# Kernel tuning notes

Hardware: AMD Instinct MI355X
Metric: run time of the kernel (lower is better)

Reference implementation:

```python
import jax, jax.numpy as jnp
import numpy as np

B, C, N, QK, VC, S = 64, 64, 256, 8, 32, 16
EPS = 1e-5
SCALE = float(np.sqrt(QK))  # qk_channel ** 0.5


def _bn(x, p):
    # eval-mode BatchNorm1d over [B, C, N]; p = [gamma, beta, mean, var]
    g, b, m, v = p
    return (x - m[None, :, None]) * (g * jax.lax.rsqrt(v + EPS))[None, :, None] + b[None, :, None]


def _conv1x1(w, x, b=None):
    y = jnp.einsum('oc,bcn->bon', w, x)
    return y if b is None else y + b[None, :, None]


def setup_inputs() -> dict:
    key = jax.random.key(0)
    ks = jax.random.split(key, 16)

    def w(k, o, i):
        return jax.random.normal(k, (o, i), jnp.float32) * (1.0 / np.sqrt(i))

    def bn_p(k, c):
        k1, k2, k3, k4 = jax.random.split(k, 4)
        return jnp.stack([
            jax.random.uniform(k1, (c,), jnp.float32) + 0.5,   # gamma
            jax.random.normal(k2, (c,), jnp.float32) * 0.1,    # beta
            jax.random.normal(k3, (c,), jnp.float32) * 0.1,    # running mean
            jax.random.uniform(k4, (c,), jnp.float32) + 0.5,   # running var (>0)
        ])

    x = jax.random.normal(ks[0], (B, C, N), jnp.float32)
    stroke_idx = jax.random.randint(ks[1], (B, N), 0, S, jnp.int32)
    stroke_idx = stroke_idx.at[:, -1].set(S - 1)  # guarantee max == S-1

    ga_q_w = w(ks[2], QK, C)
    sa_q_w = w(ks[3], QK, C)
    inp = {
        'x': x,
        'stroke_idx': stroke_idx,
        'n_strokes': S,
        'ga_q_w': ga_q_w,
        'ga_k_w': ga_q_w.copy(),  # k initialized as clone of q in source
        'ga_v_w': w(ks[4], VC, C),
        'ga_v_b': jax.random.normal(ks[5], (VC,), jnp.float32) * 0.01,
        'ga_bn_p': bn_p(ks[6], VC),
        'ga_lb_w': w(ks[7], VC, C),
        'ga_lb_bn_p': bn_p(ks[8], VC),
        'sa_q_w': sa_q_w,
        'sa_k_w': sa_q_w.copy(),
        'sa_v_w': w(ks[9], VC, C),
        'sa_v_b': jax.random.normal(ks[10], (VC,), jnp.float32) * 0.01,
        'sa_bn_p': bn_p(ks[11], VC),
        'sa_lb_w': w(ks[12], VC, C),
        'sa_lb_bn_p': bn_p(ks[13], VC),
        'mlp_w1': w(ks[14], 4 * C, C),
        'mlp_bn1_p': bn_p(jax.random.fold_in(key, 100), 4 * C),
        'mlp_w2': w(ks[15], C, 4 * C),
        'mlp_bn2_p': bn_p(jax.random.fold_in(key, 101), C),
    }
    return inp


def _ga_block(x, qw, kw, vw, vb):
    q = jnp.einsum('oc,bcn->bno', qw, x)                 # [B,N,QK]
    k = jnp.einsum('oc,bcn->bon', kw, x)                 # [B,QK,N]
    v = jnp.einsum('oc,bcn->bno', vw, x) + vb[None, None, :]  # [B,N,VC]
    attn = jax.nn.softmax(jnp.einsum('bno,bom->bnm', q, k) / SCALE, axis=-1)
    return jnp.einsum('bnm,bmv->bvn', attn, v)           # [B,VC,N]


def _sa_block(x, stroke_idx, n_strokes, qw, kw, vw, vb):
    q = jnp.einsum('oc,bcn->bno', qw, x)
    k = jnp.einsum('oc,bcn->bon', kw, x)
    v = jnp.einsum('oc,bcn->bno', vw, x) + vb[None, None, :]
    base = jnp.einsum('bno,bom->bnm', q, k) / SCALE      # [B,N,N]
    # per-stroke additive mask: 0 where stroke == i else 1e-6 (as in source)
    masks = jnp.where(stroke_idx[None, :, :] == jnp.arange(n_strokes)[:, None, None],
                      0.0, 1e-6).astype(base.dtype)       # [S,B,N]
    energy = (base[None] + masks[:, :, None, :]) * 10.0   # [S,B,N,N]
    attn = jax.nn.softmax(energy, axis=-1)
    # sum over strokes fused into the contraction
    return jnp.einsum('sbnm,bmv->bvn', attn, v)           # [B,VC,N]


def reference(x, stroke_idx, n_strokes, ga_q_w, ga_k_w, ga_v_w, ga_v_b, ga_bn_p,
              ga_lb_w, ga_lb_bn_p, sa_q_w, sa_k_w, sa_v_w, sa_v_b, sa_bn_p,
              sa_lb_w, sa_lb_bn_p, mlp_w1, mlp_bn1_p, mlp_w2, mlp_bn2_p):
    f_ga = _bn(_ga_block(x, ga_q_w, ga_k_w, ga_v_w, ga_v_b), ga_bn_p) \
         + _bn(_conv1x1(ga_lb_w, x), ga_lb_bn_p)
    f_sa = _bn(_sa_block(x, stroke_idx, n_strokes, sa_q_w, sa_k_w, sa_v_w, sa_v_b), sa_bn_p) \
         + _bn(_conv1x1(sa_lb_w, x), sa_lb_bn_p)
    f = jnp.concatenate([f_ga, f_sa], axis=1)            # [B,C,N]
    h = jax.nn.relu(_bn(_conv1x1(mlp_w1, f), mlp_bn1_p))  # [B,4C,N]
    f_mlp = _bn(_conv1x1(mlp_w2, h), mlp_bn2_p)           # [B,C,N]
    return jax.nn.relu(f_mlp + f)
```

## Files before the change

kernel.cpp:

```cpp
#include <hip/hip_runtime.h>
#include <math.h>


#define EPS    1e-5f
#define LOG2E  1.4426950408889634f

#define OFF_QGA 0u
#define OFF_KGA 131072u
#define OFF_VGA 262144u
#define OFF_QSA 786432u
#define OFF_KSA 917504u
#define OFF_VSA 1048576u
#define OFF_F   1572864u
#define OFF_H   2621440u

__global__ __launch_bounds__(512) void k_proj(
    const float* __restrict__ x,
    const float* __restrict__ gaq, const float* __restrict__ gak,
    const float* __restrict__ gav, const float* __restrict__ gavb,
    const float* __restrict__ galb, const float* __restrict__ galbbn,
    const float* __restrict__ saq, const float* __restrict__ sak,
    const float* __restrict__ sav, const float* __restrict__ savb,
    const float* __restrict__ salb, const float* __restrict__ salbbn,
    float* ws)
{
    __shared__ float O2[160][65];
    const int lane = threadIdx.x & 63;
    const int wvu  = __builtin_amdgcn_readfirstlane((int)(threadIdx.x >> 6));
    const int b    = blockIdx.x >> 2;
    const int n0   = (blockIdx.x & 3) << 6;
    const int p0g  = blockIdx.x << 6;

    float xr[64];
    const float* xb = x + (size_t)(b * 64) * 256 + n0 + lane;
    #pragma unroll
    for (int c = 0; c < 64; ++c) xr[c] = xb[c * 256];

    for (int i = 0; i < 20; ++i) {
        const int slot = wvu * 20 + i;
        const float* wr; float mul = 1.f, add = 0.f;
        if (slot < 8)        { wr = gaq + slot * 64; }
        else if (slot < 16)  { wr = gak + (slot - 8) * 64; }
        else if (slot < 48)  { int vc = slot - 16; wr = gav + vc * 64; add = gavb[vc]; }
        else if (slot < 56)  { wr = saq + (slot - 48) * 64; }
        else if (slot < 64)  { wr = sak + (slot - 56) * 64; }
        else if (slot < 96)  { int vc = slot - 64; wr = sav + vc * 64; add = savb[vc]; }
        else if (slot < 128) { int vc = slot - 96; wr = galb + vc * 64;
                               float s = galbbn[vc] * rsqrtf(galbbn[96 + vc] + EPS);
                               mul = s; add = galbbn[32 + vc] - galbbn[64 + vc] * s; }
        else                 { int vc = slot - 128; wr = salb + vc * 64;
                               float s = salbbn[vc] * rsqrtf(salbbn[96 + vc] + EPS);
                               mul = s; add = salbbn[32 + vc] - salbbn[64 + vc] * s; }
        float acc = 0.f;
        #pragma unroll
        for (int c = 0; c < 64; ++c) acc = fmaf(wr[c], xr[c], acc);
        O2[slot][lane] = acc * mul + add;
    }
    __syncthreads();

    for (int t = threadIdx.x; t < 2560; t += 512) {
        int u, rb, l; unsigned g;
        if (t < 128)       { u = t;        rb = 0;   l = 1; g = OFF_QGA; }
        else if (t < 256)  { u = t - 128;  rb = 8;   l = 1; g = OFF_KGA; }
        else if (t < 768)  { u = t - 256;  rb = 16;  l = 3; g = OFF_VGA; }
        else if (t < 896)  { u = t - 768;  rb = 48;  l = 1; g = OFF_QSA; }
        else if (t < 1024) { u = t - 896;  rb = 56;  l = 1; g = OFF_KSA; }
        else if (t < 1536) { u = t - 1024; rb = 64;  l = 3; g = OFF_VSA; }
        else               { u = t - 1536; rb = 96;  l = 4; g = OFF_F;   }
        const int p    = u >> l;
        const int off4 = u & ((1 << l) - 1);
        const int row  = rb + off4 * 4;
        float4 v;
        v.x = O2[row + 0][p]; v.y = O2[row + 1][p];
        v.z = O2[row + 2][p]; v.w = O2[row + 3][p];
        *(float4*)(ws + g + (size_t)(p0g + p) * (4u << l) + off4 * 4) = v;
    }
}

__global__ __launch_bounds__(512) void k_attn(
    const float* __restrict__ wsr, const float* __restrict__ gabnp,
    const float* __restrict__ sabnp, float* F)
{
    __shared__ float MW[8][64];
    __shared__ float ZW[8][64];
    __shared__ float AW[8][64][33];
    const int which = blockIdx.x >> 8;
    const int bb    = blockIdx.x & 255;
    const int b     = bb >> 2;
    const int n0    = (bb & 3) << 6;
    const unsigned ro = which ? 786432u : 0u;
    const float* Q = wsr + OFF_QGA + ro;
    const float* K = wsr + OFF_KGA + ro;
    const float* V = wsr + OFF_VGA + ro;
    const float* bnp = which ? sabnp : gabnp;
    const float factor   = which ? 3.5355339059327378f : 0.35355339059327378f;
    const float outscale = which ? 16.f : 1.f;
    const int   choff    = which << 5;

    const int lane = threadIdx.x & 63;
    const int w    = __builtin_amdgcn_readfirstlane((int)(threadIdx.x >> 6));
    const int p    = b * 256 + n0 + lane;
    const float fl = factor * LOG2E;
    float4 qa = *(const float4*)(Q + (size_t)p * 8);
    float4 qb = *(const float4*)(Q + (size_t)p * 8 + 4);
    qa.x *= fl; qa.y *= fl; qa.z *= fl; qa.w *= fl;
    qb.x *= fl; qb.y *= fl; qb.z *= fl; qb.w *= fl;
    const int m0 = w << 5;
    const float* Kb = K + (size_t)(b * 256 + m0) * 8;
    const float* Vb = V + (size_t)(b * 256 + m0) * 32;

    float M = -1e30f;
    #pragma unroll 4
    for (int i = 0; i < 32; ++i) {
        const float4 k0 = *(const float4*)(Kb + i * 8);
        const float4 k1 = *(const float4*)(Kb + i * 8 + 4);
        float t0 = qa.x * k0.x + qa.y * k0.y + qa.z * k0.z + qa.w * k0.w;
        float t1 = qb.x * k1.x + qb.y * k1.y + qb.z * k1.z + qb.w * k1.w;
        M = fmaxf(M, t0 + t1);
    }
    float Z = 0.f;
    float acc[32];
    #pragma unroll
    for (int j = 0; j < 32; ++j) acc[j] = 0.f;
    #pragma unroll 2
    for (int i = 0; i < 32; ++i) {
        const float4 k0 = *(const float4*)(Kb + i * 8);
        const float4 k1 = *(const float4*)(Kb + i * 8 + 4);
        float t0 = qa.x * k0.x + qa.y * k0.y + qa.z * k0.z + qa.w * k0.w;
        float t1 = qb.x * k1.x + qb.y * k1.y + qb.z * k1.z + qb.w * k1.w;
        float pv = exp2f(t0 + t1 - M);
        Z += pv;
        const float* vr = Vb + (size_t)i * 32;
        #pragma unroll
        for (int j4 = 0; j4 < 8; ++j4) {
            float4 vv = *(const float4*)(vr + j4 * 4);
            acc[j4 * 4 + 0] = fmaf(pv, vv.x, acc[j4 * 4 + 0]);
            acc[j4 * 4 + 1] = fmaf(pv, vv.y, acc[j4 * 4 + 1]);
            acc[j4 * 4 + 2] = fmaf(pv, vv.z, acc[j4 * 4 + 2]);
            acc[j4 * 4 + 3] = fmaf(pv, vv.w, acc[j4 * 4 + 3]);
        }
    }
    MW[w][lane] = M;
    ZW[w][lane] = Z;
    #pragma unroll
    for (int j = 0; j < 32; ++j) AW[w][lane][j] = acc[j];
    __syncthreads();

    const int vc = threadIdx.x & 31;
    const int rg = threadIdx.x >> 5;
    const float g  = bnp[vc], be = bnp[32 + vc], mn = bnp[64 + vc], va = bnp[96 + vc];
    const float s    = g * rsqrtf(va + EPS) * outscale;
    const float bias = be - mn * (g * rsqrtf(va + EPS));
    for (int r = 0; r < 4; ++r) {
        const int rr = rg * 4 + r;
        float Mx = MW[0][rr];
        #pragma unroll
        for (int u = 1; u < 8; ++u) Mx = fmaxf(Mx, MW[u][rr]);
        float Zt = 0.f, A = 0.f;
        #pragma unroll
        for (int u = 0; u < 8; ++u) {
            float cw = exp2f(MW[u][rr] - Mx);
            Zt += ZW[u][rr] * cw;
            A   = fmaf(AW[u][rr][vc], cw, A);
        }
        float* fp = F + (size_t)(b * 256 + n0 + rr) * 64 + choff + vc;
        *fp = (A / Zt) * s + bias + *fp;
    }
}

__global__ __launch_bounds__(256) void k_mlp1(
    const float* __restrict__ Fin, const float* __restrict__ w1,
    const float* __restrict__ bn1, float* __restrict__ H)
{
    __shared__ __align__(16) float wL[64][68];
    const int jg = blockIdx.x & 3;
    const int nt = (blockIdx.x >> 2) & 7;
    const int b  = blockIdx.x >> 5;
    const int j0 = jg << 6;
    const int n0 = nt << 5;
    for (int t = threadIdx.x; t < 4096; t += 256) {
        int jj = t >> 6, c = t & 63;
        wL[jj][c] = w1[(j0 + jj) * 64 + c];
    }
    __syncthreads();
    const int lane = threadIdx.x & 63;
    const int wq = __builtin_amdgcn_readfirstlane((int)(threadIdx.x >> 6));
    const int j  = j0 + lane;
    const int pbase = b * 256 + n0 + wq * 8;
    const float* f0 = Fin + (size_t)pbase * 64;
    float acc[8] = {0.f,0.f,0.f,0.f,0.f,0.f,0.f,0.f};
    #pragma unroll
    for (int c4 = 0; c4 < 16; ++c4) {
        float4 wv = *(const float4*)&wL[lane][c4 * 4];
        #pragma unroll
        for (int r = 0; r < 8; ++r) {
            float4 fv = *(const float4*)&f0[r * 64 + c4 * 4];
            acc[r] += wv.x * fv.x + wv.y * fv.y + wv.z * fv.z + wv.w * fv.w;
        }
    }
    const float gg = bn1[j], be = bn1[256 + j], mn = bn1[512 + j], va = bn1[768 + j];
    const float s    = gg * rsqrtf(va + EPS);
    const float bias = be - mn * s;
    #pragma unroll
    for (int r = 0; r < 8; ++r)
        H[(size_t)(pbase + r) * 256 + j] = fmaxf(acc[r] * s + bias, 0.f);
}

__global__ __launch_bounds__(256) void k_mlp2(
    const float* __restrict__ H, const float* __restrict__ w2,
    const float* __restrict__ bn2, const float* __restrict__ Fin,
    float* __restrict__ out)
{
    __shared__ __align__(16) float w2L[64][268];
    __shared__ float OT[64][33];
    const int b   = blockIdx.x >> 3;
    const int nw  = (blockIdx.x & 7) << 5;
    for (int t = threadIdx.x; t < 16384; t += 256) {
        w2L[t >> 8][t & 255] = w2[t];
    }
    __syncthreads();
    const int lane = threadIdx.x & 63;
    const int wq = __builtin_amdgcn_readfirstlane((int)(threadIdx.x >> 6));
    const float g = bn2[lane], be = bn2[64 + lane], mn = bn2[128 + lane], va = bn2[192 + lane];
    const float s    = g * rsqrtf(va + EPS);
    const float bias = be - mn * s;
    for (int g2 = 0; g2 < 2; ++g2) {
        const int nl = wq * 8 + g2 * 4;
        const int pb = b * 256 + nw + nl;
        const float* h0 = H + (size_t)pb * 256;
        float acc[4] = {0.f,0.f,0.f,0.f};
        for (int j4 = 0; j4 < 64; ++j4) {
            float4 wv = *(const float4*)&w2L[lane][j4 * 4];
            #pragma unroll
            for (int r = 0; r < 4; ++r) {
                float4 hv = *(const float4*)&h0[r * 256 + j4 * 4];
                acc[r] += wv.x * hv.x + wv.y * hv.y + wv.z * hv.z + wv.w * hv.w;
            }
        }
        #pragma unroll
        for (int r = 0; r < 4; ++r) {
            float f = Fin[(size_t)(pb + r) * 64 + lane];
            OT[lane][nl + r] = fmaxf(acc[r] * s + bias + f, 0.f);
        }
    }
    __syncthreads();
    for (int t = threadIdx.x; t < 512; t += 256) {
        int c = t >> 3, j4 = (t & 7) << 2;
        float4 v;
        v.x = OT[c][j4]; v.y = OT[c][j4 + 1]; v.z = OT[c][j4 + 2]; v.w = OT[c][j4 + 3];
        *(float4*)(out + (size_t)(b * 64 + c) * 256 + nw + j4) = v;
    }
}

extern "C" void kernel_launch(void* const* d_in, const int* in_sizes, int n_in,
                              void* d_out, int out_size, void* d_ws, size_t ws_size,
                              hipStream_t stream) {
    const float* x      = (const float*)d_in[0];
    const float* gaq    = (const float*)d_in[3];
    const float* gak    = (const float*)d_in[4];
    const float* gav    = (const float*)d_in[5];
    const float* gavb   = (const float*)d_in[6];
    const float* gabnp  = (const float*)d_in[7];
    const float* galb   = (const float*)d_in[8];
    const float* galbbn = (const float*)d_in[9];
    const float* saq    = (const float*)d_in[10];
    const float* sak    = (const float*)d_in[11];
    const float* sav    = (const float*)d_in[12];
    const float* savb   = (const float*)d_in[13];
    const float* sabnp  = (const float*)d_in[14];
    const float* salb   = (const float*)d_in[15];
    const float* salbbn = (const float*)d_in[16];
    const float* w1     = (const float*)d_in[17];
    const float* bn1    = (const float*)d_in[18];
    const float* w2     = (const float*)d_in[19];
    const float* bn2    = (const float*)d_in[20];
    float* ws   = (float*)d_ws;
    float* outp = (float*)d_out;

    k_proj<<<dim3(256), dim3(512), 0, stream>>>(
        x, gaq, gak, gav, gavb, galb, galbbn,
        saq, sak, sav, savb, salb, salbbn, ws);

    k_attn<<<dim3(512), dim3(512), 0, stream>>>(ws, gabnp, sabnp, ws + OFF_F);

    k_mlp1<<<dim3(2048), dim3(256), 0, stream>>>(ws + OFF_F, w1, bn1, ws + OFF_H);
    k_mlp2<<<dim3(512),  dim3(256), 0, stream>>>(ws + OFF_H, w2, bn2, ws + OFF_F, outp);
}
```

Baseline: 181.0 us.

## Stage weights, K/V, F and H tiles in LDS across all four kernels

Every kernel now stages its operands in shared memory before computing. The projection weights and BN scale/bias go to LDS, K and V for the batch are loaded cooperatively in the attention kernel, and F and H tiles are loaded in the MLP kernels instead of each lane reading global memory. The attention kernel now computes the global row max across waves first and reduces partial sums with LDS atomics, which removes the rescale merge and the second QK pass by keeping scores in registers. k_mlp2 moves to 512 threads with one row group per wave. The larger LDS footprint (especially w2L plus hT in k_mlp2) and the extra register pressure can lower occupancy.

After: 211.0 us. +16.6%, slower.

```diff
diff --git a/kernel.cpp b/kernel.cpp
--- a/kernel.cpp
+++ b/kernel.cpp
@@ -24,41 +24,62 @@
     const float* __restrict__ salb, const float* __restrict__ salbbn,
     float* ws)
 {
+    __shared__ __align__(16) float wLDS[160][68];
     __shared__ float O2[160][65];
-    const int lane = threadIdx.x & 63;
-    const int wvu  = __builtin_amdgcn_readfirstlane((int)(threadIdx.x >> 6));
+    __shared__ float mulL[160], addL[160];
+    const int tid  = threadIdx.x;
+    const int lane = tid & 63;
+    const int wvu  = __builtin_amdgcn_readfirstlane((int)(tid >> 6));
     const int b    = blockIdx.x >> 2;
     const int n0   = (blockIdx.x & 3) << 6;
     const int p0g  = blockIdx.x << 6;
 
+    for (int t = tid; t < 10240; t += 512) {
+        int slot = t >> 6, c = t & 63;
+        const float* src; int r;
+        if (slot < 8)        { src = gaq;  r = slot; }
+        else if (slot < 16)  { src = gak;  r = slot - 8; }
+        else if (slot < 48)  { src = gav;  r = slot - 16; }
+        else if (slot < 56)  { src = saq;  r = slot - 48; }
+        else if (slot < 64)  { src = sak;  r = slot - 56; }
+        else if (slot < 96)  { src = sav;  r = slot - 64; }
+        else if (slot < 128) { src = galb; r = slot - 96; }
+        else                 { src = salb; r = slot - 128; }
+        wLDS[slot][c] = src[r * 64 + c];
+    }
+    if (tid < 160) {
+        int slot = tid; float mul = 1.f, add = 0.f;
+        if (slot >= 16 && slot < 48)       { add = gavb[slot - 16]; }
+        else if (slot >= 64 && slot < 96)  { add = savb[slot - 64]; }
+        else if (slot >= 96 && slot < 128) { int vc = slot - 96;
+            float s = galbbn[vc] * rsqrtf(galbbn[96 + vc] + EPS);
+            mul = s; add = galbbn[32 + vc] - galbbn[64 + vc] * s; }
+        else if (slot >= 128)              { int vc = slot - 128;
+            float s = salbbn[vc] * rsqrtf(salbbn[96 + vc] + EPS);
+            mul = s; add = salbbn[32 + vc] - salbbn[64 + vc] * s; }
+        mulL[slot] = mul; addL[slot] = add;
+    }
+
     float xr[64];
     const float* xb = x + (size_t)(b * 64) * 256 + n0 + lane;
     #pragma unroll
     for (int c = 0; c < 64; ++c) xr[c] = xb[c * 256];
+    __syncthreads();
 
     for (int i = 0; i < 20; ++i) {
         const int slot = wvu * 20 + i;
-        const float* wr; float mul = 1.f, add = 0.f;
-        if (slot < 8)        { wr = gaq + slot * 64; }
-        else if (slot < 16)  { wr = gak + (slot - 8) * 64; }
-        else if (slot < 48)  { int vc = slot - 16; wr = gav + vc * 64; add = gavb[vc]; }
-        else if (slot < 56)  { wr = saq + (slot - 48) * 64; }
-        else if (slot < 64)  { wr = sak + (slot - 56) * 64; }
-        else if (slot < 96)  { int vc = slot - 64; wr = sav + vc * 64; add = savb[vc]; }
-        else if (slot < 128) { int vc = slot - 96; wr = galb + vc * 64;
-                               float s = galbbn[vc] * rsqrtf(galbbn[96 + vc] + EPS);
-                               mul = s; add = galbbn[32 + vc] - galbbn[64 + vc] * s; }
-        else                 { int vc = slot - 128; wr = salb + vc * 64;
-                               float s = salbbn[vc] * rsqrtf(salbbn[96 + vc] + EPS);
-                               mul = s; add = salbbn[32 + vc] - salbbn[64 + vc] * s; }
         float acc = 0.f;
         #pragma unroll
-        for (int c = 0; c < 64; ++c) acc = fmaf(wr[c], xr[c], acc);
-        O2[slot][lane] = acc * mul + add;
-    }
-    __syncthreads();
-
-    for (int t = threadIdx.x; t < 2560; t += 512) {
+        for (int c4 = 0; c4 < 16; ++c4) {
+            float4 wv = *(const float4*)&wLDS[slot][c4 * 4];
+            acc += wv.x * xr[c4 * 4] + wv.y * xr[c4 * 4 + 1]
+                 + wv.z * xr[c4 * 4 + 2] + wv.w * xr[c4 * 4 + 3];
+        }
+        O2[slot][lane] = acc * mulL[slot] + addL[slot];
+    }
+    __syncthreads();
+
+    for (int t = tid; t < 2560; t += 512) {
         int u, rb, l; unsigned g;
         if (t < 128)       { u = t;        rb = 0;   l = 1; g = OFF_QGA; }
         else if (t < 256)  { u = t - 128;  rb = 8;   l = 1; g = OFF_KGA; }
@@ -81,24 +102,37 @@
     const float* __restrict__ wsr, const float* __restrict__ gabnp,
     const float* __restrict__ sabnp, float* F)
 {
+    __shared__ __align__(16) float KL[256][8];
+    __shared__ __align__(16) float VL[256][32];
     __shared__ float MW[8][64];
-    __shared__ float ZW[8][64];
-    __shared__ float AW[8][64][33];
+    __shared__ float AW[64][33];
+    __shared__ float ZW[64];
+    const int tid   = threadIdx.x;
     const int which = blockIdx.x >> 8;
     const int bb    = blockIdx.x & 255;
     const int b     = bb >> 2;
     const int n0    = (bb & 3) << 6;
     const unsigned ro = which ? 786432u : 0u;
     const float* Q = wsr + OFF_QGA + ro;
-    const float* K = wsr + OFF_KGA + ro;
-    const float* V = wsr + OFF_VGA + ro;
     const float* bnp = which ? sabnp : gabnp;
     const float factor   = which ? 3.5355339059327378f : 0.35355339059327378f;
     const float outscale = which ? 16.f : 1.f;
     const int   choff    = which << 5;
 
-    const int lane = threadIdx.x & 63;
-    const int w    = __builtin_amdgcn_readfirstlane((int)(threadIdx.x >> 6));
+    {
+        const float4* Kg = (const float4*)(wsr + OFF_KGA + ro + (size_t)b * 2048);
+        const float4* Vg = (const float4*)(wsr + OFF_VGA + ro + (size_t)b * 8192);
+        ((float4*)KL)[tid] = Kg[tid];
+        #pragma unroll
+        for (int t = 0; t < 4; ++t)
+            ((float4*)VL)[tid + t * 512] = Vg[tid + t * 512];
+        for (int t = tid; t < 2176; t += 512) {
+            if (t < 2112) ((float*)AW)[t] = 0.f; else ZW[t - 2112] = 0.f;
+        }
+    }
+
+    const int lane = tid & 63;
+    const int w    = __builtin_amdgcn_readfirstlane((int)(tid >> 6));
     const int p    = b * 256 + n0 + lane;
     const float fl = factor * LOG2E;
     float4 qa = *(const float4*)(Q + (size_t)p * 8);
@@ -106,63 +140,57 @@
     qa.x *= fl; qa.y *= fl; qa.z *= fl; qa.w *= fl;
     qb.x *= fl; qb.y *= fl; qb.z *= fl; qb.w *= fl;
     const int m0 = w << 5;
-    const float* Kb = K + (size_t)(b * 256 + m0) * 8;
-    const float* Vb = V + (size_t)(b * 256 + m0) * 32;
-
+    __syncthreads();
+
+    float tv[32];
     float M = -1e30f;
-    #pragma unroll 4
+    #pragma unroll
     for (int i = 0; i < 32; ++i) {
-        const float4 k0 = *(const float4*)(Kb + i * 8);
-        const float4 k1 = *(const float4*)(Kb + i * 8 + 4);
-        float t0 = qa.x * k0.x + qa.y * k0.y + qa.z * k0.z + qa.w * k0.w;
-        float t1 = qb.x * k1.x + qb.y * k1.y + qb.z * k1.z + qb.w * k1.w;
-        M = fmaxf(M, t0 + t1);
-    }
+        float4 k0 = *(const float4*)&KL[m0 + i][0];
+        float4 k1 = *(const float4*)&KL[m0 + i][4];
+        tv[i] = qa.x * k0.x + qa.y * k0.y + qa.z * k0.z + qa.w * k0.w
+              + qb.x * k1.x + qb.y * k1.y + qb.z * k1.z + qb.w * k1.w;
+        M = fmaxf(M, tv[i]);
+    }
+    MW[w][lane] = M;
+    __syncthreads();
+    float Mx = MW[0][lane];
+    #pragma unroll
+    for (int u = 1; u < 8; ++u) Mx = fmaxf(Mx, MW[u][lane]);
+
     float Z = 0.f;
     float acc[32];
     #pragma unroll
     for (int j = 0; j < 32; ++j) acc[j] = 0.f;
-    #pragma unroll 2
+    #pragma unroll
     for (int i = 0; i < 32; ++i) {
-        const float4 k0 = *(const float4*)(Kb + i * 8);
-        const float4 k1 = *(const float4*)(Kb + i * 8 + 4);
-        float t0 = qa.x * k0.x + qa.y * k0.y + qa.z * k0.z + qa.w * k0.w;
-        float t1 = qb.x * k1.x + qb.y * k1.y + qb.z * k1.z + qb.w * k1.w;
-        float pv = exp2f(t0 + t1 - M);
+        float pv = exp2f(tv[i] - Mx);
         Z += pv;
-        const float* vr = Vb + (size_t)i * 32;
         #pragma unroll
         for (int j4 = 0; j4 < 8; ++j4) {
-            float4 vv = *(const float4*)(vr + j4 * 4);
+            float4 vv = *(const float4*)&VL[m0 + i][j4 * 4];
             acc[j4 * 4 + 0] = fmaf(pv, vv.x, acc[j4 * 4 + 0]);
             acc[j4 * 4 + 1] = fmaf(pv, vv.y, acc[j4 * 4 + 1]);
             acc[j4 * 4 + 2] = fmaf(pv, vv.z, acc[j4 * 4 + 2]);
             acc[j4 * 4 + 3] = fmaf(pv, vv.w, acc[j4 * 4 + 3]);
         }
     }
-    MW[w][lane] = M;
-    ZW[w][lane] = Z;
-    #pragma unroll
-    for (int j = 0; j < 32; ++j) AW[w][lane][j] = acc[j];
-    __syncthreads();
-
-    const int vc = threadIdx.x & 31;
-    const int rg = threadIdx.x >> 5;
+    atomicAdd(&ZW[lane], Z);
+    #pragma unroll
+    for (int j = 0; j < 32; ++j) atomicAdd(&AW[lane][j], acc[j]);
+    __syncthreads();
+
+    const int vc = tid & 31;
+    const int rg = tid >> 5;
     const float g  = bnp[vc], be = bnp[32 + vc], mn = bnp[64 + vc], va = bnp[96 + vc];
-    const float s    = g * rsqrtf(va + EPS) * outscale;
-    const float bias = be - mn * (g * rsqrtf(va + EPS));
+    const float sf   = g * rsqrtf(va + EPS);
+    const float s    = sf * outscale;
+    const float bias = be - mn * sf;
+    #pragma unroll
     for (int r = 0; r < 4; ++r) {
         const int rr = rg * 4 + r;
-        float Mx = MW[0][rr];
-        #pragma unroll
-        for (int u = 1; u < 8; ++u) Mx = fmaxf(Mx, MW[u][rr]);
-        float Zt = 0.f, A = 0.f;
-        #pragma unroll
-        for (int u = 0; u < 8; ++u) {
-            float cw = exp2f(MW[u][rr] - Mx);
-            Zt += ZW[u][rr] * cw;
-            A   = fmaf(AW[u][rr][vc], cw, A);
-        }
+        float A  = AW[rr][vc];
+        float Zt = ZW[rr];
         float* fp = F + (size_t)(b * 256 + n0 + rr) * 64 + choff + vc;
         *fp = (A / Zt) * s + bias + *fp;
     }
@@ -173,6 +201,7 @@
     const float* __restrict__ bn1, float* __restrict__ H)
 {
     __shared__ __align__(16) float wL[64][68];
+    __shared__ __align__(16) float fL[32][68];
     const int jg = blockIdx.x & 3;
     const int nt = (blockIdx.x >> 2) & 7;
     const int b  = blockIdx.x >> 5;
@@ -182,19 +211,27 @@
         int jj = t >> 6, c = t & 63;
         wL[jj][c] = w1[(j0 + jj) * 64 + c];
     }
+    {
+        const float4* Fg = (const float4*)(Fin + (size_t)(b * 256 + n0) * 64);
+        #pragma unroll
+        for (int t = 0; t < 2; ++t) {
+            int u = threadIdx.x + t * 256;
+            int pp = u >> 4, c4 = u & 15;
+            *(float4*)&fL[pp][c4 * 4] = Fg[u];
+        }
+    }
     __syncthreads();
     const int lane = threadIdx.x & 63;
     const int wq = __builtin_amdgcn_readfirstlane((int)(threadIdx.x >> 6));
     const int j  = j0 + lane;
     const int pbase = b * 256 + n0 + wq * 8;
-    const float* f0 = Fin + (size_t)pbase * 64;
     float acc[8] = {0.f,0.f,0.f,0.f,0.f,0.f,0.f,0.f};
     #pragma unroll
     for (int c4 = 0; c4 < 16; ++c4) {
         float4 wv = *(const float4*)&wL[lane][c4 * 4];
         #pragma unroll
         for (int r = 0; r < 8; ++r) {
-            float4 fv = *(const float4*)&f0[r * 64 + c4 * 4];
+            float4 fv = *(const float4*)&fL[wq * 8 + r][c4 * 4];
             acc[r] += wv.x * fv.x + wv.y * fv.y + wv.z * fv.z + wv.w * fv.w;
         }
     }
@@ -206,17 +243,27 @@
         H[(size_t)(pbase + r) * 256 + j] = fmaxf(acc[r] * s + bias, 0.f);
 }
 
-__global__ __launch_bounds__(256) void k_mlp2(
+__global__ __launch_bounds__(512) void k_mlp2(
     const float* __restrict__ H, const float* __restrict__ w2,
     const float* __restrict__ bn2, const float* __restrict__ Fin,
     float* __restrict__ out)
 {
     __shared__ __align__(16) float w2L[64][268];
+    __shared__ __align__(16) float hT[32][260];
     __shared__ float OT[64][33];
     const int b   = blockIdx.x >> 3;
     const int nw  = (blockIdx.x & 7) << 5;
-    for (int t = threadIdx.x; t < 16384; t += 256) {
+    for (int t = threadIdx.x; t < 16384; t += 512) {
         w2L[t >> 8][t & 255] = w2[t];
+    }
+    {
+        const float4* Hg = (const float4*)(H + (size_t)(b * 256 + nw) * 256);
+        #pragma unroll
+        for (int t = 0; t < 4; ++t) {
+            int u = threadIdx.x + t * 512;
+            int pp = u >> 6, c4 = u & 63;
+            *(float4*)&hT[pp][c4 * 4] = Hg[u];
+        }
     }
     __syncthreads();
     const int lane = threadIdx.x & 63;
@@ -224,27 +271,26 @@
     const float g = bn2[lane], be = bn2[64 + lane], mn = bn2[128 + lane], va = bn2[192 + lane];
     const float s    = g * rsqrtf(va + EPS);
     const float bias = be - mn * s;
-    for (int g2 = 0; g2 < 2; ++g2) {
-        const int nl = wq * 8 + g2 * 4;
-        const int pb = b * 256 + nw + nl;
-        const float* h0 = H + (size_t)pb * 256;
-        float acc[4] = {0.f,0.f,0.f,0.f};
-        for (int j4 = 0; j4 < 64; ++j4) {
-            float4 wv = *(const float4*)&w2L[lane][j4 * 4];
-            #pragma unroll
-            for (int r = 0; r < 4; ++r) {
-                float4 hv = *(const float4*)&h0[r * 256 + j4 * 4];
-                acc[r] += wv.x * hv.x + wv.y * hv.y + wv.z * hv.z + wv.w * hv.w;
-            }
-        }
+    const int nl = wq * 4;
+    float acc[4] = {0.f,0.f,0.f,0.f};
+    #pragma unroll 8
+    for (int j4 = 0; j4 < 64; ++j4) {
+        float4 wv = *(const float4*)&w2L[lane][j4 * 4];
         #pragma unroll
         for (int r = 0; r < 4; ++r) {
-            float f = Fin[(size_t)(pb + r) * 64 + lane];
-            OT[lane][nl + r] = fmaxf(acc[r] * s + bias + f, 0.f);
-        }
-    }
-    __syncthreads();
-    for (int t = threadIdx.x; t < 512; t += 256) {
+            float4 hv = *(const float4*)&hT[nl + r][j4 * 4];
+            acc[r] += wv.x * hv.x + wv.y * hv.y + wv.z * hv.z + wv.w * hv.w;
+        }
+    }
+    const int pb = b * 256 + nw + nl;
+    #pragma unroll
+    for (int r = 0; r < 4; ++r) {
+        float f = Fin[(size_t)(pb + r) * 64 + lane];
+        OT[lane][nl + r] = fmaxf(acc[r] * s + bias + f, 0.f);
+    }
+    __syncthreads();
+    {
+        int t = threadIdx.x;
         int c = t >> 3, j4 = (t & 7) << 2;
         float4 v;
         v.x = OT[c][j4]; v.y = OT[c][j4 + 1]; v.z = OT[c][j4 + 2]; v.w = OT[c][j4 + 3];
@@ -284,5 +330,5 @@
     k_attn<<<dim3(512), dim3(512), 0, stream>>>(ws, gabnp, sabnp, ws + OFF_F);
 
     k_mlp1<<<dim3(2048), dim3(256), 0, stream>>>(ws + OFF_F, w1, bn1, ws + OFF_H);
-    k_mlp2<<<dim3(512),  dim3(256), 0, stream>>>(ws + OFF_H, w2, bn2, ws + OFF_F, outp);
-}
+    k_mlp2<<<dim3(512),  dim3(512), 0, stream>>>(ws + OFF_H, w2, bn2, ws + OFF_F, outp);
+}
```
